# Kernel tuning notes

Measured on AMD Instinct MI355X. Metric: run time of the kernel, lower is better.

The kernel has to match this reference:

```python
import jax, jax.numpy as jnp
import numpy as np

EMB = 512
N_MODELS = 5
HID = 64
N_Q = 2048
N_P = 256


def setup_inputs() -> dict:
    key = jax.random.key(0)
    ks = jax.random.split(key, 6)
    return {
        "query_features": jax.random.normal(ks[0], (N_Q, EMB), dtype=jnp.float32),
        "prototypes": jax.random.normal(ks[1], (N_P, EMB), dtype=jnp.float32),
        # first Linear: weight [64, 2*EMB], bias [64], per model
        "W1": jax.random.normal(ks[2], (N_MODELS, HID, 2 * EMB), dtype=jnp.float32) * 0.02,
        "b1": jax.random.normal(ks[3], (N_MODELS, HID), dtype=jnp.float32) * 0.02,
        # second Linear: weight [1, 64] -> stored as [64], bias scalar per model
        "W2": jax.random.normal(ks[4], (N_MODELS, HID), dtype=jnp.float32) * 0.02,
        "b2": jax.random.normal(ks[5], (N_MODELS,), dtype=jnp.float32) * 0.02,
    }


def reference(query_features, prototypes, W1, b1, W2, b2):
    d = query_features.shape[1]
    # cat([q_i, p_j]) @ W1^T == q_i @ W1[:, :d]^T + p_j @ W1[:, d:]^T
    W1q = W1[:, :, :d]   # [M, H, d]
    W1p = W1[:, :, d:]   # [M, H, d]
    hq = jnp.einsum('qd,mhd->mqh', query_features, W1q)  # [M, Q, H]
    hp = jnp.einsum('pd,mhd->mph', prototypes, W1p)      # [M, P, H]
    h = jax.nn.relu(hq[:, :, None, :] + hp[:, None, :, :] + b1[:, None, None, :])  # [M, Q, P, H]
    out = jnp.einsum('mqph,mh->mqp', h, W2) + b2[:, None, None]  # [M, Q, P]
    mean_d = out.mean(axis=0)
    # torch.std default is unbiased (ddof=1)
    unc = jnp.std(out, axis=0, ddof=1)
    return mean_d * jnp.exp(-unc)
```

## Files before the change

kernel.cpp:

```cpp
#include <hip/hip_runtime.h>
#include <math.h>

#define EMB 512
#define NM 5
#define HID 64
#define NQ 2048
#define NP 256

typedef __attribute__((ext_vector_type(8))) short short8;
typedef __attribute__((ext_vector_type(4))) short short4s;
typedef __attribute__((ext_vector_type(4))) float floatx4;
typedef __attribute__((ext_vector_type(4))) float vf4;
typedef __attribute__((ext_vector_type(2))) float vf2;

#define A_BY  0u
#define B_BY  2621440u
#define WH_BY 2949120u
#define WL_BY 3604480u
#define QH_BY 4259840u
#define PH_BY 6356992u

#define LST 72

__device__ inline unsigned short bfr(float f) {
    unsigned u = __float_as_uint(f);
    u += 0x7FFFu + ((u >> 16) & 1u);
    return (unsigned short)(u >> 16);
}

__global__ __launch_bounds__(256) void cvt_pre(const float* __restrict__ Q,
                                               const float* __restrict__ P,
                                               const float* __restrict__ W1,
                                               short* __restrict__ WHg,
                                               short* __restrict__ WLg,
                                               short* __restrict__ QHg,
                                               short* __restrict__ PHg) {
    int i = blockIdx.x * 256 + threadIdx.x;
    if (i < 81920) {
        float4 v = ((const float4*)W1)[i];
        short4s hi, lo;
#define C1(I, V) { unsigned short h_ = bfr(V); hi[I] = (short)h_; \
    lo[I] = (short)bfr((V) - __uint_as_float(((unsigned)h_) << 16)); }
        C1(0, v.x) C1(1, v.y) C1(2, v.z) C1(3, v.w)
#undef C1
        ((short4s*)WHg)[i] = hi;
        ((short4s*)WLg)[i] = lo;
    } else if (i < 81920 + 262144) {
        int j = i - 81920;
        float4 v = ((const float4*)Q)[j];
        short4s hi;
        hi[0] = (short)bfr(v.x); hi[1] = (short)bfr(v.y);
        hi[2] = (short)bfr(v.z); hi[3] = (short)bfr(v.w);
        ((short4s*)QHg)[j] = hi;
    } else {
        int j = i - 344064;
        float4 v = ((const float4*)P)[j];
        short4s hi;
        hi[0] = (short)bfr(v.x); hi[1] = (short)bfr(v.y);
        hi[2] = (short)bfr(v.z); hi[3] = (short)bfr(v.w);
        ((short4s*)PHg)[j] = hi;
    }
}

__global__ __launch_bounds__(256) void gemm_v4(const short* __restrict__ WHg,
                                               const short* __restrict__ WLg,
                                               const short* __restrict__ QHg,
                                               const short* __restrict__ PHg,
                                               const float* __restrict__ b1,
                                               float* __restrict__ A,
                                               float* __restrict__ Bv) {
    __shared__ short XH[2][16 * LST];
    __shared__ short WH[2][64 * LST];
    __shared__ short WL[2][64 * LST];

    int tid  = threadIdx.x;
    int lane = tid & 63;
    int ht   = tid >> 6;
    int m    = blockIdx.x % 5;
    int rt   = blockIdx.x / 5;
    int r0   = rt * 16;
    bool isQ = rt < 128;

    int wrow = tid >> 3;
    int wg8  = (tid & 7) * 8;
    int off  = isQ ? 0 : 512;
    const short* whp0 = WHg + ((size_t)(m * 64 + wrow)) * 1024 + off + wg8;
    const short* whp1 = whp0 + 32 * 1024;
    const short* wlp0 = WLg + ((size_t)(m * 64 + wrow)) * 1024 + off + wg8;
    const short* wlp1 = wlp0 + 32 * 1024;
    bool hasX = tid < 128;
    int xrow  = tid >> 3;
    const short* xp = (isQ ? QHg + (size_t)(r0 + xrow) * 512
                           : PHg + (size_t)(r0 - NQ + xrow) * 512) + wg8;

    int arix = (lane & 15) * LST + (lane >> 4) * 8;
    int brix = (ht * 16 + (lane & 15)) * LST + (lane >> 4) * 8;

    floatx4 ac = {0, 0, 0, 0};
    short8 wh0, wh1, wl0, wl1, xh;

    wh0 = *(const short8*)&whp0[0]; wh1 = *(const short8*)&whp1[0];
    wl0 = *(const short8*)&wlp0[0]; wl1 = *(const short8*)&wlp1[0];
    if (hasX) xh = *(const short8*)&xp[0];
    *(short8*)&WH[0][wrow * LST + wg8] = wh0;
    *(short8*)&WH[0][(wrow + 32) * LST + wg8] = wh1;
    *(short8*)&WL[0][wrow * LST + wg8] = wl0;
    *(short8*)&WL[0][(wrow + 32) * LST + wg8] = wl1;
    if (hasX) *(short8*)&XH[0][xrow * LST + wg8] = xh;

#pragma unroll 1
    for (int c = 0; c < 8; ++c) {
        int cur = c & 1;
        if (c < 7) {
            int k0 = (c + 1) * 64;
            wh0 = *(const short8*)&whp0[k0]; wh1 = *(const short8*)&whp1[k0];
            wl0 = *(const short8*)&wlp0[k0]; wl1 = *(const short8*)&wlp1[k0];
            if (hasX) xh = *(const short8*)&xp[k0];
        }
        __syncthreads();

#pragma unroll
        for (int s = 0; s < 2; ++s) {
            short8 Ah = *(const short8*)&XH[cur][arix + s * 32];
            short8 Bh = *(const short8*)&WH[cur][brix + s * 32];
            short8 Bl = *(const short8*)&WL[cur][brix + s * 32];
            ac = __builtin_amdgcn_mfma_f32_16x16x32_bf16(Ah, Bl, ac, 0, 0, 0);
            ac = __builtin_amdgcn_mfma_f32_16x16x32_bf16(Ah, Bh, ac, 0, 0, 0);
        }

        if (c < 7) {
            int nb = cur ^ 1;
            *(short8*)&WH[nb][wrow * LST + wg8] = wh0;
            *(short8*)&WH[nb][(wrow + 32) * LST + wg8] = wh1;
            *(short8*)&WL[nb][wrow * LST + wg8] = wl0;
            *(short8*)&WL[nb][(wrow + 32) * LST + wg8] = wl1;
            if (hasX) *(short8*)&XH[nb][xrow * LST + wg8] = xh;
        }
    }

    int col  = lane & 15;
    int rloc = (lane >> 4) * 4;
    int hh   = ht * 16 + col;
    int rr   = r0 + rloc;

    if (isQ) {
        float bb = b1[m * 64 + hh];
        float* dst = &A[((size_t)m * NQ + rr) * HID + hh];
        dst[0 * HID] = ac.x + bb; dst[1 * HID] = ac.y + bb;
        dst[2 * HID] = ac.z + bb; dst[3 * HID] = ac.w + bb;
    } else {
        int p = rr - NQ;
        float* dst = &Bv[(((size_t)(m * 16 + (hh >> 2))) * NP + p) * 4 + (hh & 3)];
        dst[0 * 4] = ac.x; dst[1 * 4] = ac.y; dst[2 * 4] = ac.z; dst[3 * 4] = ac.w;
    }
}

__global__ __launch_bounds__(256, 4) void fused_main(const float* __restrict__ A,
                                                     const float* __restrict__ Bv,
                                                     const float* __restrict__ W2,
                                                     const float* __restrict__ b2,
                                                     float* __restrict__ out) {
    int p  = threadIdx.x;
    int q0 = blockIdx.x * 4;

    const vf4* Bq = (const vf4*)Bv + p;

    float s1[4] = {0.f, 0.f, 0.f, 0.f}, s2[4] = {0.f, 0.f, 0.f, 0.f};
    vf4 Bc[16];

#pragma unroll 1
    for (int m = 0; m < NM; ++m) {
#pragma unroll
        for (int j = 0; j < 16; ++j) Bc[j] = Bq[(m * 16 + j) * NP];

        const float* Ar = A + ((size_t)m * NQ + q0) * HID;
        const float* Wm = W2 + m * HID;
        float bb = b2[m];

#pragma unroll
        for (int qi = 0; qi < 4; ++qi) {
            const float* Aq = Ar + qi * HID;
            vf2 acc = {0.f, 0.f};
#pragma unroll
            for (int j = 0; j < 16; ++j) {
                vf2 a0 = *(const vf2*)&Aq[j * 4 + 0];
                vf2 a1 = *(const vf2*)&Aq[j * 4 + 2];
                vf2 w0 = *(const vf2*)&Wm[j * 4 + 0];
                vf2 w1 = *(const vf2*)&Wm[j * 4 + 2];
                vf2 z  = {0.f, 0.f};
                vf2 t0 = __builtin_elementwise_max(a0 + Bc[j].xy, z);
                vf2 t1 = __builtin_elementwise_max(a1 + Bc[j].zw, z);
                acc = t0 * w0 + acc;
                acc = t1 * w1 + acc;
            }
            float x = acc.x + acc.y + bb;
            s1[qi] += x;
            s2[qi] = fmaf(x, x, s2[qi]);
        }
    }

#pragma unroll
    for (int qi = 0; qi < 4; ++qi) {
        float mean = s1[qi] * 0.2f;
        float var  = fmaxf((s2[qi] - s1[qi] * s1[qi] * 0.2f) * 0.25f, 0.f);
        out[(size_t)(q0 + qi) * NP + p] = mean * __expf(-sqrtf(var));
    }
}

extern "C" void kernel_launch(void* const* d_in, const int* in_sizes, int n_in,
                              void* d_out, int out_size, void* d_ws, size_t ws_size,
                              hipStream_t stream) {
    const float* Q  = (const float*)d_in[0];
    const float* P  = (const float*)d_in[1];
    const float* W1 = (const float*)d_in[2];
    const float* b1 = (const float*)d_in[3];
    const float* W2 = (const float*)d_in[4];
    const float* b2 = (const float*)d_in[5];
    float* out = (float*)d_out;

    char*  ws  = (char*)d_ws;
    float* A   = (float*)(ws + A_BY);
    float* B   = (float*)(ws + B_BY);
    short* WHg = (short*)(ws + WH_BY);
    short* WLg = (short*)(ws + WL_BY);
    short* QHg = (short*)(ws + QH_BY);
    short* PHg = (short*)(ws + PH_BY);

    cvt_pre<<<1472, 256, 0, stream>>>(Q, P, W1, WHg, WLg, QHg, PHg);
    gemm_v4<<<720, 256, 0, stream>>>(WHg, WLg, QHg, PHg, b1, A, B);
    fused_main<<<512, 256, 0, stream>>>(A, B, W2, b2, out);
}
```

Measured before the change: 106.4 us.

## Stage A rows in shared memory and retile fused_main to 8q x 64p blocks

```diff
diff --git a/kernel.cpp b/kernel.cpp
--- a/kernel.cpp
+++ b/kernel.cpp
@@ -155,36 +155,52 @@
     }
 }
 
-__global__ __launch_bounds__(256, 4) void fused_main(const float* __restrict__ A,
-                                                     const float* __restrict__ Bv,
-                                                     const float* __restrict__ W2,
-                                                     const float* __restrict__ b2,
-                                                     float* __restrict__ out) {
-    int p  = threadIdx.x;
-    int q0 = blockIdx.x * 4;
-
-    const vf4* Bq = (const vf4*)Bv + p;
-
-    float s1[4] = {0.f, 0.f, 0.f, 0.f}, s2[4] = {0.f, 0.f, 0.f, 0.f};
-    vf4 Bc[16];
+#define AST 68
+__global__ __launch_bounds__(256) void fused_main(const float* __restrict__ A,
+                                                  const float* __restrict__ Bv,
+                                                  const float* __restrict__ W2,
+                                                  const float* __restrict__ b2,
+                                                  float* __restrict__ out) {
+    __shared__ float As[NM][8][AST];
+
+    int tid  = threadIdx.x;
+    int bp   = (blockIdx.x & 3) * 64;
+    int q0   = (blockIdx.x >> 2) * 8;
+    int p    = tid >> 2;
+    int qg   = tid & 3;
+
+    {
+        const float4* Ag = (const float4*)A;
+        for (int i = tid; i < 640; i += 256) {
+            int m = i >> 7, rem = i & 127;
+            int qr = rem >> 4, j = rem & 15;
+            *(float4*)&As[m][qr][j * 4] =
+                Ag[(size_t)m * (NQ * 16) + (size_t)(q0 + qr) * 16 + j];
+        }
+    }
+    __syncthreads();
+
+    const vf4* Bq = (const vf4*)Bv + (bp + p);
+
+    float s1[2] = {0.f, 0.f}, s2[2] = {0.f, 0.f};
 
 #pragma unroll 1
     for (int m = 0; m < NM; ++m) {
+        vf4 Bc[16];
 #pragma unroll
         for (int j = 0; j < 16; ++j) Bc[j] = Bq[(m * 16 + j) * NP];
 
-        const float* Ar = A + ((size_t)m * NQ + q0) * HID;
         const float* Wm = W2 + m * HID;
         float bb = b2[m];
 
 #pragma unroll
-        for (int qi = 0; qi < 4; ++qi) {
-            const float* Aq = Ar + qi * HID;
+        for (int qi = 0; qi < 2; ++qi) {
+            const float* Ar = &As[m][qg * 2 + qi][0];
             vf2 acc = {0.f, 0.f};
 #pragma unroll
             for (int j = 0; j < 16; ++j) {
-                vf2 a0 = *(const vf2*)&Aq[j * 4 + 0];
-                vf2 a1 = *(const vf2*)&Aq[j * 4 + 2];
+                vf2 a0 = *(const vf2*)&Ar[j * 4 + 0];
+                vf2 a1 = *(const vf2*)&Ar[j * 4 + 2];
                 vf2 w0 = *(const vf2*)&Wm[j * 4 + 0];
                 vf2 w1 = *(const vf2*)&Wm[j * 4 + 2];
                 vf2 z  = {0.f, 0.f};
@@ -200,10 +216,11 @@
     }
 
 #pragma unroll
-    for (int qi = 0; qi < 4; ++qi) {
+    for (int qi = 0; qi < 2; ++qi) {
         float mean = s1[qi] * 0.2f;
         float var  = fmaxf((s2[qi] - s1[qi] * s1[qi] * 0.2f) * 0.25f, 0.f);
-        out[(size_t)(q0 + qi) * NP + p] = mean * __expf(-sqrtf(var));
+        out[(size_t)(q0 + qg * 2 + qi) * NP + bp + p] =
+            mean * __expf(-sqrtf(var));
     }
 }
 
@@ -228,5 +245,5 @@
 
     cvt_pre<<<1472, 256, 0, stream>>>(Q, P, W1, WHg, WLg, QHg, PHg);
     gemm_v4<<<720, 256, 0, stream>>>(WHg, WLg, QHg, PHg, b1, A, B);
-    fused_main<<<512, 256, 0, stream>>>(A, B, W2, b2, out);
-}
+    fused_main<<<1024, 256, 0, stream>>>(A, B, W2, b2, out);
+}
```

New measurement: 94.87 us. 1.12x faster.

## Retile fused_main to 64 prototypes x 8 queries per block with halved B register cache

Applied to the files above, without the earlier changes.

```diff
diff --git a/kernel.cpp b/kernel.cpp
--- a/kernel.cpp
+++ b/kernel.cpp
@@ -155,55 +155,71 @@
     }
 }
 
-__global__ __launch_bounds__(256, 4) void fused_main(const float* __restrict__ A,
-                                                     const float* __restrict__ Bv,
-                                                     const float* __restrict__ W2,
-                                                     const float* __restrict__ b2,
-                                                     float* __restrict__ out) {
-    int p  = threadIdx.x;
-    int q0 = blockIdx.x * 4;
+__global__ __launch_bounds__(256) void fused_main(const float* __restrict__ A,
+                                                  const float* __restrict__ Bv,
+                                                  const float* __restrict__ W2,
+                                                  const float* __restrict__ b2,
+                                                  float* __restrict__ out) {
+    int tid  = threadIdx.x;
+    int lane = tid & 63;
+    int wq   = tid >> 6;
+    int bp   = (blockIdx.x & 3) * 64;
+    int q0   = (blockIdx.x >> 2) * 8;
+    int p    = bp + lane;
+    int qa   = q0 + wq * 2;
 
     const vf4* Bq = (const vf4*)Bv + p;
 
-    float s1[4] = {0.f, 0.f, 0.f, 0.f}, s2[4] = {0.f, 0.f, 0.f, 0.f};
-    vf4 Bc[16];
+    float s1[2] = {0.f, 0.f}, s2[2] = {0.f, 0.f};
 
 #pragma unroll 1
     for (int m = 0; m < NM; ++m) {
-#pragma unroll
-        for (int j = 0; j < 16; ++j) Bc[j] = Bq[(m * 16 + j) * NP];
-
-        const float* Ar = A + ((size_t)m * NQ + q0) * HID;
+        float bb = b2[m];
+        const float* A0 = A + ((size_t)m * NQ + qa) * HID;
+        const float* A1 = A0 + HID;
         const float* Wm = W2 + m * HID;
-        float bb = b2[m];
-
-#pragma unroll
-        for (int qi = 0; qi < 4; ++qi) {
-            const float* Aq = Ar + qi * HID;
-            vf2 acc = {0.f, 0.f};
-#pragma unroll
-            for (int j = 0; j < 16; ++j) {
-                vf2 a0 = *(const vf2*)&Aq[j * 4 + 0];
-                vf2 a1 = *(const vf2*)&Aq[j * 4 + 2];
-                vf2 w0 = *(const vf2*)&Wm[j * 4 + 0];
-                vf2 w1 = *(const vf2*)&Wm[j * 4 + 2];
+
+        vf2 acc0 = {0.f, 0.f}, acc1 = {0.f, 0.f};
+
+#pragma unroll
+        for (int jh = 0; jh < 2; ++jh) {
+            vf4 Bc[8];
+#pragma unroll
+            for (int j = 0; j < 8; ++j)
+                Bc[j] = Bq[(m * 16 + jh * 8 + j) * NP];
+
+#pragma unroll
+            for (int j = 0; j < 8; ++j) {
+                int h0 = (jh * 8 + j) * 4;
+                vf2 w0 = *(const vf2*)&Wm[h0 + 0];
+                vf2 w1 = *(const vf2*)&Wm[h0 + 2];
                 vf2 z  = {0.f, 0.f};
-                vf2 t0 = __builtin_elementwise_max(a0 + Bc[j].xy, z);
-                vf2 t1 = __builtin_elementwise_max(a1 + Bc[j].zw, z);
-                acc = t0 * w0 + acc;
-                acc = t1 * w1 + acc;
+                vf2 a00 = *(const vf2*)&A0[h0 + 0];
+                vf2 a01 = *(const vf2*)&A0[h0 + 2];
+                vf2 t00 = __builtin_elementwise_max(a00 + Bc[j].xy, z);
+                vf2 t01 = __builtin_elementwise_max(a01 + Bc[j].zw, z);
+                acc0 = t00 * w0 + acc0;
+                acc0 = t01 * w1 + acc0;
+                vf2 a10 = *(const vf2*)&A1[h0 + 0];
+                vf2 a11 = *(const vf2*)&A1[h0 + 2];
+                vf2 t10 = __builtin_elementwise_max(a10 + Bc[j].xy, z);
+                vf2 t11 = __builtin_elementwise_max(a11 + Bc[j].zw, z);
+                acc1 = t10 * w0 + acc1;
+                acc1 = t11 * w1 + acc1;
             }
-            float x = acc.x + acc.y + bb;
-            s1[qi] += x;
-            s2[qi] = fmaf(x, x, s2[qi]);
-        }
-    }
-
-#pragma unroll
-    for (int qi = 0; qi < 4; ++qi) {
+        }
+
+        float x0 = acc0.x + acc0.y + bb;
+        s1[0] += x0; s2[0] = fmaf(x0, x0, s2[0]);
+        float x1 = acc1.x + acc1.y + bb;
+        s1[1] += x1; s2[1] = fmaf(x1, x1, s2[1]);
+    }
+
+#pragma unroll
+    for (int qi = 0; qi < 2; ++qi) {
         float mean = s1[qi] * 0.2f;
         float var  = fmaxf((s2[qi] - s1[qi] * s1[qi] * 0.2f) * 0.25f, 0.f);
-        out[(size_t)(q0 + qi) * NP + p] = mean * __expf(-sqrtf(var));
+        out[(size_t)(qa + qi) * NP + p] = mean * __expf(-sqrtf(var));
     }
 }
 
@@ -228,5 +244,5 @@
 
     cvt_pre<<<1472, 256, 0, stream>>>(Q, P, W1, WHg, WLg, QHg, PHg);
     gemm_v4<<<720, 256, 0, stream>>>(WHg, WLg, QHg, PHg, b1, A, B);
-    fused_main<<<512, 256, 0, stream>>>(A, B, W2, b2, out);
-}
+    fused_main<<<1024, 256, 0, stream>>>(A, B, W2, b2, out);
+}
```

Result: no change. 106.4 us (-0.1%).
